# Kernel optimization log

Hardware: AMD Instinct MI355X
Metric: run time of the kernel (lower is better)

## Reference

```python
import jax, jax.numpy as jnp
import numpy as np

SIGMA = 1.0
NUM_CLASSES = 10


def setup_inputs() -> dict:
    key = jax.random.key(0)
    k1, k2, k3, k4 = jax.random.split(key, 4)
    ns, nt, d = 4096, 4096, 256
    return {
        "source_feature": jax.random.normal(k1, (ns, d), dtype=jnp.float32),
        "source_label": jax.random.randint(k2, (ns,), 0, NUM_CLASSES),
        "target_feature": jax.random.normal(k3, (nt, d), dtype=jnp.float32),
        "class_weight": jax.random.uniform(k4, (NUM_CLASSES,), dtype=jnp.float32),
    }


def _rbf_gram(x, y, sigma):
    # K[i, j] = exp(-||x_i - y_j||^2 / (2*sigma)); [n, m]
    x2 = jnp.sum(x * x, axis=-1)  # [n]
    y2 = jnp.sum(y * y, axis=-1)  # [m]
    sq = x2[:, None] + y2[None, :] - 2.0 * (x @ y.T)
    sq = jnp.maximum(sq, 0.0)
    return jnp.exp(-sq / (2.0 * sigma))


def reference(source_feature, source_label, target_feature, class_weight):
    ns = source_feature.shape[0]
    nt = target_feature.shape[0]
    w = class_weight[source_label]          # [ns] per-sample weight
    n = jnp.sum(w)                          # weighted source count

    Kss = _rbf_gram(source_feature, source_feature, SIGMA)  # [ns, ns]
    Ktt = _rbf_gram(target_feature, target_feature, SIGMA)  # [nt, nt]
    Kst = _rbf_gram(source_feature, target_feature, SIGMA)  # [ns, nt]

    first = jnp.einsum('i,ij,j->', w, Kss, w)
    sec = jnp.sum(Ktt)
    third = jnp.einsum('i,ij->', w, Kst)

    return first / (n * n) + sec / (nt * nt) - 2.0 * third / (n * nt)
```

## Files before the change

kernel.cpp:

```cpp
#include <hip/hip_runtime.h>
#include <hip/hip_bf16.h>


typedef float f32x4 __attribute__((ext_vector_type(4)));

#define D 256

static __device__ __forceinline__ unsigned char f32_to_e4m3(float f) {
    unsigned int u = __float_as_uint(f);
    unsigned int sg = (u >> 24) & 0x80;
    unsigned int um = u & 0x7FFFFFFF;
    unsigned int r = um + 0x0007FFFF + ((um >> 20) & 1);
    int e8 = (int)((r >> 23) & 0xFF) - 127 + 7;
    unsigned int m8 = (r >> 20) & 7;
    if (e8 <= 0) return (unsigned char)sg;
    if (e8 > 15 || (e8 == 15 && m8 == 7))
        return (unsigned char)(sg | 0x7E);
    return (unsigned char)(sg | ((unsigned)e8 << 3) | m8);
}


__global__ __launch_bounds__(256) void prep_kernel(
    const float* __restrict__ sf, const float* __restrict__ tf,
    const int* __restrict__ lbl, const float* __restrict__ cw,
    unsigned char* __restrict__ sfb, unsigned char* __restrict__ tfb,
    float* __restrict__ x2s, float* __restrict__ x2t,
    float* __restrict__ wv, int ns)
{
    int row = blockIdx.x * 4 + (threadIdx.x >> 6);
    int t = threadIdx.x & 63;
    bool is_src = row < ns;
    int r = is_src ? row : row - ns;
    const float* src = (is_src ? sf : tf) + (size_t)r * D;
    unsigned char* dstb = is_src ? sfb : tfb;

    float4 v = ((const float4*)src)[t];
    uchar4 q;
    q.x = f32_to_e4m3(v.x); q.y = f32_to_e4m3(v.y);
    q.z = f32_to_e4m3(v.z); q.w = f32_to_e4m3(v.w);

    int g = r >> 4, rr = r & 15;
    int s_ = t >> 3;
    int kg = (t >> 1) & 3;
    int j0 = (t & 1) * 4;
    size_t idx = ((size_t)(g * 8 + s_) * 512) + (size_t)(rr + 16 * kg) * 8 + j0;
    *(uchar4*)(dstb + idx) = q;

    float s = v.x * v.x + v.y * v.y + v.z * v.z + v.w * v.w;
    #pragma unroll
    for (int o = 32; o; o >>= 1) s += __shfl_xor(s, o);

    if (t == 0) {
        if (is_src) { wv[r] = cw[lbl[r]]; x2s[r] = s; }
        else        { x2t[r] = s; }
    }
}

__global__ __launch_bounds__(256, 3) void gram_kernel(
    const unsigned char* __restrict__ sfb, const unsigned char* __restrict__ tfb,
    const float* __restrict__ x2s, const float* __restrict__ x2t,
    const float* __restrict__ wv, float* __restrict__ bout,
    int ti_s, int ti_t)
{
    int tri_s = ti_s * (ti_s + 1) / 2;
    int tri_t = ti_t * (ti_t + 1) / 2;
    int blk = blockIdx.x;

    int mode, bi, bj;
    const unsigned char *X, *Y;
    const float *x2xp, *x2yp;
    if (blk < tri_s + tri_t) {
        int T, idx;
        if (blk < tri_s) { mode = 0; idx = blk; T = ti_s; X = sfb; Y = sfb; x2xp = x2s; x2yp = x2s; }
        else { mode = 1; idx = blk - tri_s; T = ti_t; X = tfb; Y = tfb; x2xp = x2t; x2yp = x2t; }
        bi = (int)((2.0f * T + 1.0f -
                    sqrtf((float)((2 * T + 1) * (2 * T + 1) - 8 * idx))) * 0.5f);
        if (bi < 0) bi = 0;
        if (bi > T - 1) bi = T - 1;
        int base = bi * (2 * T - bi + 1) / 2;
        while (base > idx) { --bi; base = bi * (2 * T - bi + 1) / 2; }
        while (idx >= base + (T - bi)) { base += (T - bi); ++bi; }
        bj = bi + (idx - base);
    } else {
        int idx = blk - tri_s - tri_t;
        mode = 2; bi = idx / ti_t; bj = idx % ti_t;
        X = sfb; Y = tfb; x2xp = x2s; x2yp = x2t;
    }
    float factor = (mode != 2 && bi != bj) ? 2.0f : 1.0f;

    int wid = threadIdx.x >> 6;
    int lane = threadIdx.x & 63;
    int wr = wid >> 1, wc = wid & 1;
    int R0 = bi * 128 + wr * 64;
    int C0 = bj * 128 + wc * 64;

    const unsigned char* XA = X + (size_t)(R0 >> 4) * 4096 + lane * 8;
    const unsigned char* YB = Y + (size_t)(C0 >> 4) * 4096 + lane * 8;

    f32x4 acc[4][4] = {};
    long af[4][4], bf_[4][4];
    #pragma unroll
    for (int sp = 0; sp < 3; ++sp) {
        #pragma unroll
        for (int m = 0; m < 4; ++m) {
            af[sp][m]  = *(const long*)(XA + (size_t)(m * 8 + sp) * 512);
            bf_[sp][m] = *(const long*)(YB + (size_t)(m * 8 + sp) * 512);
        }
    }
    #pragma unroll
    for (int s = 0; s < 8; ++s) {
        const int cur = s & 3;
        if (s < 5) {
            const int pf = (s + 3) & 3;
            #pragma unroll
            for (int m = 0; m < 4; ++m) {
                af[pf][m]  = *(const long*)(XA + (size_t)(m * 8 + s + 3) * 512);
                bf_[pf][m] = *(const long*)(YB + (size_t)(m * 8 + s + 3) * 512);
            }
        }
        #pragma unroll
        for (int m = 0; m < 4; ++m)
            #pragma unroll
            for (int n = 0; n < 4; ++n)
                acc[m][n] = __builtin_amdgcn_mfma_f32_16x16x32_fp8_fp8(
                    af[cur][m], bf_[cur][n], acc[m][n], 0, 0, 0);
    }

    int crow = (lane >> 4) * 4;
    int ccol = lane & 15;
    float x2yc[4];
    #pragma unroll
    for (int n = 0; n < 4; ++n) x2yc[n] = x2yp[C0 + 16 * n + ccol];

    float s = 0.0f;
    #pragma unroll
    for (int m = 0; m < 4; ++m) {
        #pragma unroll
        for (int r = 0; r < 4; ++r) {
            int gr = R0 + 16 * m + crow + r;
            float rx2 = x2xp[gr];
            float sq0 = fmaxf(rx2 + x2yc[0] - 2.0f * acc[m][0][r], 0.0f);
            float sq1 = fmaxf(rx2 + x2yc[1] - 2.0f * acc[m][1][r], 0.0f);
            float sq2 = fmaxf(rx2 + x2yc[2] - 2.0f * acc[m][2][r], 0.0f);
            float sq3 = fmaxf(rx2 + x2yc[3] - 2.0f * acc[m][3][r], 0.0f);
            float mn = fminf(fminf(sq0, sq1), fminf(sq2, sq3));
            if (__any(mn < 180.0f)) {
                float rw = (mode != 1) ? wv[gr] : 1.0f;
                float sqv[4] = {sq0, sq1, sq2, sq3};
                #pragma unroll
                for (int n = 0; n < 4; ++n) {
                    int gc = C0 + 16 * n + ccol;
                    float K = __expf(-0.5f * sqv[n]);
                    if (mode != 2 && gr == gc) K = 0.0f;
                    float wf = (mode == 0) ? rw * wv[gc] : rw;
                    s += wf * K;
                }
            }
        }
    }
    s *= factor;
    #pragma unroll
    for (int o = 32; o; o >>= 1) s += __shfl_xor(s, o);

    __shared__ float bsum[4];
    if (lane == 0) bsum[wid] = s;
    __syncthreads();
    if (threadIdx.x == 0)
        bout[blk] = (bsum[0] + bsum[1]) + (bsum[2] + bsum[3]);
}

__global__ __launch_bounds__(1024) void reduce_kernel(
    const float* __restrict__ wv, int ns,
    const float* __restrict__ bout, int tri_s, int tri_t, int nb,
    float* __restrict__ out, int nt)
{
    int tid = threadIdx.x;
    float n = 0.0f, dsq = 0.0f, a0 = 0.0f, a1 = 0.0f, a2 = 0.0f;
    for (int i = tid; i < ns; i += 1024) {
        float w = wv[i];
        n += w;
        dsq += w * w;
    }
    for (int i = tid; i < nb; i += 1024) {
        float v = bout[i];
        if (i < tri_s) a0 += v;
        else if (i < tri_s + tri_t) a1 += v;
        else a2 += v;
    }
    #pragma unroll
    for (int o = 32; o; o >>= 1) {
        n   += __shfl_xor(n, o);
        dsq += __shfl_xor(dsq, o);
        a0  += __shfl_xor(a0, o);
        a1  += __shfl_xor(a1, o);
        a2  += __shfl_xor(a2, o);
    }
    __shared__ float ln[16], ld[16], l0[16], l1[16], l2[16];
    int w = tid >> 6;
    if ((tid & 63) == 0) { ln[w] = n; ld[w] = dsq; l0[w] = a0; l1[w] = a1; l2[w] = a2; }
    __syncthreads();
    if (tid == 0) {
        float N = 0, DQ = 0, A0 = 0, A1 = 0, A2 = 0;
        #pragma unroll
        for (int i = 0; i < 16; ++i) {
            N += ln[i]; DQ += ld[i]; A0 += l0[i]; A1 += l1[i]; A2 += l2[i];
        }
        float fnt = (float)nt;
        out[0] = (A0 + DQ) / (N * N) + (A1 + fnt) / (fnt * fnt)
               - 2.0f * A2 / (N * fnt);
    }
}

extern "C" void kernel_launch(void* const* d_in, const int* in_sizes, int n_in,
                              void* d_out, int out_size, void* d_ws, size_t ws_size,
                              hipStream_t stream) {
    const float* sf = (const float*)d_in[0];
    const int* lbl = (const int*)d_in[1];
    const float* tf = (const float*)d_in[2];
    const float* cw = (const float*)d_in[3];
    float* out = (float*)d_out;

    int ns = in_sizes[1];
    int d = in_sizes[0] / ns;
    int nt = in_sizes[2] / d;

    char* p = (char*)d_ws;
    unsigned char* sfb = (unsigned char*)p;  p += (size_t)ns * d;
    unsigned char* tfb = (unsigned char*)p;  p += (size_t)nt * d;
    float* x2s = (float*)p;                  p += (size_t)ns * sizeof(float);
    float* x2t = (float*)p;                  p += (size_t)nt * sizeof(float);
    float* wv  = (float*)p;                  p += (size_t)ns * sizeof(float);
    float* bout = (float*)p;

    prep_kernel<<<(ns + nt) / 4, 256, 0, stream>>>(sf, tf, lbl, cw, sfb, tfb,
                                                   x2s, x2t, wv, ns);

    int ti_s = ns / 128, ti_t = nt / 128;
    int tri_s = ti_s * (ti_s + 1) / 2;
    int tri_t = ti_t * (ti_t + 1) / 2;
    int nblocks = tri_s + tri_t + ti_s * ti_t;
    gram_kernel<<<nblocks, 256, 0, stream>>>(sfb, tfb, x2s, x2t, wv, bout,
                                             ti_s, ti_t);

    reduce_kernel<<<1, 1024, 0, stream>>>(wv, ns, bout, tri_s, tri_t, nblocks,
                                          out, nt);
}
```

Measured before the change: 41.76 us.

## Batch gram tiles per block with XCD-aware mapping and wider fp8 loads

The gram kernel now processes four consecutive 128x128 tiles per block, assigned through an XCD-aware remap so neighbouring tiles share an XCD's L2. Per-mode partial sums go to a 3-wide output array. The fp8 packed layout is changed so each lane loads 16 bytes per step, halving the number of global load instructions. The prep kernel stages a 16-row group in LDS and writes it out with coalesced nontemporal 16-byte stores. The aims are to cut launch and tail overhead, raise cache reuse, and reduce load instruction count. The cost is fewer blocks (about 2080 → 520), which may lower occupancy and load balance.

```diff
diff --git a/kernel.cpp b/kernel.cpp
--- a/kernel.cpp
+++ b/kernel.cpp
@@ -3,20 +3,21 @@
 
 
 typedef float f32x4 __attribute__((ext_vector_type(4)));
+typedef long long2v __attribute__((ext_vector_type(2)));
+typedef unsigned int u32x4 __attribute__((ext_vector_type(4)));
 
 #define D 256
 
-static __device__ __forceinline__ unsigned char f32_to_e4m3(float f) {
+static __device__ __forceinline__ unsigned int f32_to_e4m3(float f) {
     unsigned int u = __float_as_uint(f);
     unsigned int sg = (u >> 24) & 0x80;
     unsigned int um = u & 0x7FFFFFFF;
     unsigned int r = um + 0x0007FFFF + ((um >> 20) & 1);
     int e8 = (int)((r >> 23) & 0xFF) - 127 + 7;
     unsigned int m8 = (r >> 20) & 7;
-    if (e8 <= 0) return (unsigned char)sg;
-    if (e8 > 15 || (e8 == 15 && m8 == 7))
-        return (unsigned char)(sg | 0x7E);
-    return (unsigned char)(sg | ((unsigned)e8 << 3) | m8);
+    if (e8 <= 0) return sg;
+    if (e8 > 15 || (e8 == 15 && m8 == 7)) return sg | 0x7E;
+    return sg | ((unsigned)e8 << 3) | m8;
 }
 
 
@@ -27,52 +28,65 @@
     float* __restrict__ x2s, float* __restrict__ x2t,
     float* __restrict__ wv, int ns)
 {
-    int row = blockIdx.x * 4 + (threadIdx.x >> 6);
-    int t = threadIdx.x & 63;
-    bool is_src = row < ns;
-    int r = is_src ? row : row - ns;
-    const float* src = (is_src ? sf : tf) + (size_t)r * D;
-    unsigned char* dstb = is_src ? sfb : tfb;
-
-    float4 v = ((const float4*)src)[t];
-    uchar4 q;
-    q.x = f32_to_e4m3(v.x); q.y = f32_to_e4m3(v.y);
-    q.z = f32_to_e4m3(v.z); q.w = f32_to_e4m3(v.w);
-
-    int g = r >> 4, rr = r & 15;
-    int s_ = t >> 3;
-    int kg = (t >> 1) & 3;
-    int j0 = (t & 1) * 4;
-    size_t idx = ((size_t)(g * 8 + s_) * 512) + (size_t)(rr + 16 * kg) * 8 + j0;
-    *(uchar4*)(dstb + idx) = q;
-
-    float s = v.x * v.x + v.y * v.y + v.z * v.z + v.w * v.w;
+    __shared__ unsigned int ldsb[1024];
+
+    int gb = blockIdx.x;
+    int nsg = ns >> 4;
+    bool is_src = gb < nsg;
+    int gloc = is_src ? gb : gb - nsg;
+    const float* src = (is_src ? sf : tf) + (size_t)gloc * 16 * D;
+    unsigned char* dstb = (is_src ? sfb : tfb) + (size_t)gloc * 4096;
+
+    int tid = threadIdx.x;
+    int l = tid & 63;
+    int w = tid >> 6;
+
+    if (is_src && tid < 16) {
+        int r = gloc * 16 + tid;
+        wv[r] = cw[lbl[r]];
+    }
+
     #pragma unroll
-    for (int o = 32; o; o >>= 1) s += __shfl_xor(s, o);
-
-    if (t == 0) {
-        if (is_src) { wv[r] = cw[lbl[r]]; x2s[r] = s; }
-        else        { x2t[r] = s; }
-    }
-}
-
-__global__ __launch_bounds__(256, 3) void gram_kernel(
-    const unsigned char* __restrict__ sfb, const unsigned char* __restrict__ tfb,
-    const float* __restrict__ x2s, const float* __restrict__ x2t,
-    const float* __restrict__ wv, float* __restrict__ bout,
-    int ti_s, int ti_t)
+    for (int p = 0; p < 4; ++p) {
+        int row = 4 * p + w;
+        int k0 = l * 4;
+        float4 v = *(const float4*)(src + row * D + k0);
+        unsigned int packed = f32_to_e4m3(v.x)
+                            | (f32_to_e4m3(v.y) << 8)
+                            | (f32_to_e4m3(v.z) << 16)
+                            | (f32_to_e4m3(v.w) << 24);
+        int s  = k0 >> 5;
+        int kg = (k0 >> 3) & 3;
+        int off = (s >> 1) * 1024 + (row + 16 * kg) * 16 + (s & 1) * 8 + (k0 & 7);
+        ldsb[off >> 2] = packed;
+
+        float ps = v.x * v.x + v.y * v.y + v.z * v.z + v.w * v.w;
+        #pragma unroll
+        for (int o = 32; o; o >>= 1) ps += __shfl_xor(ps, o);
+        if (l == 0) {
+            int gr = gloc * 16 + row;
+            if (is_src) x2s[gr] = ps; else x2t[gr] = ps;
+        }
+    }
+    __syncthreads();
+    u32x4 val = ((const u32x4*)ldsb)[tid];
+    __builtin_nontemporal_store(val, ((u32x4*)dstb) + tid);
+}
+
+static __device__ __forceinline__ void decode_tile(
+    int blk, int ti_s, int ti_t,
+    const unsigned char* sfb, const unsigned char* tfb,
+    const float* x2s, const float* x2t,
+    int& mode, int& bi, int& bj,
+    const unsigned char*& X, const unsigned char*& Y,
+    const float*& x2x, const float*& x2y, float& factor)
 {
     int tri_s = ti_s * (ti_s + 1) / 2;
     int tri_t = ti_t * (ti_t + 1) / 2;
-    int blk = blockIdx.x;
-
-    int mode, bi, bj;
-    const unsigned char *X, *Y;
-    const float *x2xp, *x2yp;
     if (blk < tri_s + tri_t) {
         int T, idx;
-        if (blk < tri_s) { mode = 0; idx = blk; T = ti_s; X = sfb; Y = sfb; x2xp = x2s; x2yp = x2s; }
-        else { mode = 1; idx = blk - tri_s; T = ti_t; X = tfb; Y = tfb; x2xp = x2t; x2yp = x2t; }
+        if (blk < tri_s) { mode = 0; idx = blk; T = ti_s; X = sfb; Y = sfb; x2x = x2s; x2y = x2s; }
+        else { mode = 1; idx = blk - tri_s; T = ti_t; X = tfb; Y = tfb; x2x = x2t; x2y = x2t; }
         bi = (int)((2.0f * T + 1.0f -
                     sqrtf((float)((2 * T + 1) * (2 * T + 1) - 8 * idx))) * 0.5f);
         if (bi < 0) bi = 0;
@@ -84,94 +98,126 @@
     } else {
         int idx = blk - tri_s - tri_t;
         mode = 2; bi = idx / ti_t; bj = idx % ti_t;
-        X = sfb; Y = tfb; x2xp = x2s; x2yp = x2t;
-    }
-    float factor = (mode != 2 && bi != bj) ? 2.0f : 1.0f;
+        X = sfb; Y = tfb; x2x = x2s; x2y = x2t;
+    }
+    factor = (mode != 2 && bi != bj) ? 2.0f : 1.0f;
+}
+
+__global__ __launch_bounds__(256, 3) void gram_kernel(
+    const unsigned char* __restrict__ sfb, const unsigned char* __restrict__ tfb,
+    const float* __restrict__ x2s, const float* __restrict__ x2t,
+    const float* __restrict__ wv, float* __restrict__ bout,
+    int ti_s, int ti_t, int NT, int NB, int TPB)
+{
+    int orig = blockIdx.x;
+    int q = NB >> 3, rm = NB & 7, xcd = orig & 7, of = orig >> 3;
+    int lb = (xcd < rm ? xcd * (q + 1) : rm * (q + 1) + (xcd - rm) * q) + of;
+    int tbeg = lb * TPB;
+    int tend = min(tbeg + TPB, NT);
 
     int wid = threadIdx.x >> 6;
     int lane = threadIdx.x & 63;
     int wr = wid >> 1, wc = wid & 1;
-    int R0 = bi * 128 + wr * 64;
-    int C0 = bj * 128 + wc * 64;
-
-    const unsigned char* XA = X + (size_t)(R0 >> 4) * 4096 + lane * 8;
-    const unsigned char* YB = Y + (size_t)(C0 >> 4) * 4096 + lane * 8;
-
-    f32x4 acc[4][4] = {};
-    long af[4][4], bf_[4][4];
-    #pragma unroll
-    for (int sp = 0; sp < 3; ++sp) {
-        #pragma unroll
-        for (int m = 0; m < 4; ++m) {
-            af[sp][m]  = *(const long*)(XA + (size_t)(m * 8 + sp) * 512);
-            bf_[sp][m] = *(const long*)(YB + (size_t)(m * 8 + sp) * 512);
-        }
-    }
-    #pragma unroll
-    for (int s = 0; s < 8; ++s) {
-        const int cur = s & 3;
-        if (s < 5) {
-            const int pf = (s + 3) & 3;
-            #pragma unroll
-            for (int m = 0; m < 4; ++m) {
-                af[pf][m]  = *(const long*)(XA + (size_t)(m * 8 + s + 3) * 512);
-                bf_[pf][m] = *(const long*)(YB + (size_t)(m * 8 + s + 3) * 512);
-            }
-        }
-        #pragma unroll
-        for (int m = 0; m < 4; ++m)
-            #pragma unroll
-            for (int n = 0; n < 4; ++n)
-                acc[m][n] = __builtin_amdgcn_mfma_f32_16x16x32_fp8_fp8(
-                    af[cur][m], bf_[cur][n], acc[m][n], 0, 0, 0);
-    }
-
     int crow = (lane >> 4) * 4;
     int ccol = lane & 15;
-    float x2yc[4];
-    #pragma unroll
-    for (int n = 0; n < 4; ++n) x2yc[n] = x2yp[C0 + 16 * n + ccol];
-
-    float s = 0.0f;
-    #pragma unroll
-    for (int m = 0; m < 4; ++m) {
-        #pragma unroll
-        for (int r = 0; r < 4; ++r) {
-            int gr = R0 + 16 * m + crow + r;
-            float rx2 = x2xp[gr];
-            float sq0 = fmaxf(rx2 + x2yc[0] - 2.0f * acc[m][0][r], 0.0f);
-            float sq1 = fmaxf(rx2 + x2yc[1] - 2.0f * acc[m][1][r], 0.0f);
-            float sq2 = fmaxf(rx2 + x2yc[2] - 2.0f * acc[m][2][r], 0.0f);
-            float sq3 = fmaxf(rx2 + x2yc[3] - 2.0f * acc[m][3][r], 0.0f);
-            float mn = fminf(fminf(sq0, sq1), fminf(sq2, sq3));
-            if (__any(mn < 180.0f)) {
-                float rw = (mode != 1) ? wv[gr] : 1.0f;
-                float sqv[4] = {sq0, sq1, sq2, sq3};
+
+    float s0 = 0.0f, s1 = 0.0f, s2 = 0.0f;
+
+    for (int t = tbeg; t < tend; ++t) {
+        int mode, bi, bj; float factor;
+        const unsigned char *X, *Y; const float *x2xp, *x2yp;
+        decode_tile(t, ti_s, ti_t, sfb, tfb, x2s, x2t,
+                    mode, bi, bj, X, Y, x2xp, x2yp, factor);
+
+        int R0 = bi * 128 + wr * 64;
+        int C0 = bj * 128 + wc * 64;
+        const unsigned char* XA = X + (size_t)(R0 >> 4) * 4096 + lane * 16;
+        const unsigned char* YB = Y + (size_t)(C0 >> 4) * 4096 + lane * 16;
+
+        f32x4 acc[4][4] = {};
+        long2v a2[2][4], b2[2][4];
+        #pragma unroll
+        for (int m = 0; m < 4; ++m) {
+            a2[0][m] = *(const long2v*)(XA + m * 4096);
+            b2[0][m] = *(const long2v*)(YB + m * 4096);
+        }
+        #pragma unroll
+        for (int ss = 0; ss < 4; ++ss) {
+            const int cur = ss & 1;
+            if (ss < 3) {
                 #pragma unroll
-                for (int n = 0; n < 4; ++n) {
-                    int gc = C0 + 16 * n + ccol;
-                    float K = __expf(-0.5f * sqv[n]);
-                    if (mode != 2 && gr == gc) K = 0.0f;
-                    float wf = (mode == 0) ? rw * wv[gc] : rw;
-                    s += wf * K;
+                for (int m = 0; m < 4; ++m) {
+                    a2[cur ^ 1][m] = *(const long2v*)(XA + m * 4096 + (ss + 1) * 1024);
+                    b2[cur ^ 1][m] = *(const long2v*)(YB + m * 4096 + (ss + 1) * 1024);
                 }
             }
-        }
-    }
-    s *= factor;
+            #pragma unroll
+            for (int m = 0; m < 4; ++m)
+                #pragma unroll
+                for (int n = 0; n < 4; ++n)
+                    acc[m][n] = __builtin_amdgcn_mfma_f32_16x16x32_fp8_fp8(
+                        a2[cur][m][0], b2[cur][n][0], acc[m][n], 0, 0, 0);
+            #pragma unroll
+            for (int m = 0; m < 4; ++m)
+                #pragma unroll
+                for (int n = 0; n < 4; ++n)
+                    acc[m][n] = __builtin_amdgcn_mfma_f32_16x16x32_fp8_fp8(
+                        a2[cur][m][1], b2[cur][n][1], acc[m][n], 0, 0, 0);
+        }
+
+        float x2yc[4];
+        #pragma unroll
+        for (int n = 0; n < 4; ++n) x2yc[n] = x2yp[C0 + 16 * n + ccol];
+
+        float s = 0.0f;
+        #pragma unroll
+        for (int m = 0; m < 4; ++m) {
+            #pragma unroll
+            for (int r = 0; r < 4; ++r) {
+                int gr = R0 + 16 * m + crow + r;
+                float rx2 = x2xp[gr];
+                float sq0 = fmaxf(rx2 + x2yc[0] - 2.0f * acc[m][0][r], 0.0f);
+                float sq1 = fmaxf(rx2 + x2yc[1] - 2.0f * acc[m][1][r], 0.0f);
+                float sq2 = fmaxf(rx2 + x2yc[2] - 2.0f * acc[m][2][r], 0.0f);
+                float sq3 = fmaxf(rx2 + x2yc[3] - 2.0f * acc[m][3][r], 0.0f);
+                float mn = fminf(fminf(sq0, sq1), fminf(sq2, sq3));
+                if (__any(mn < 180.0f)) {
+                    float rw = (mode != 1) ? wv[gr] : 1.0f;
+                    float sqv[4] = {sq0, sq1, sq2, sq3};
+                    #pragma unroll
+                    for (int n = 0; n < 4; ++n) {
+                        int gc = C0 + 16 * n + ccol;
+                        float K = __expf(-0.5f * sqv[n]);
+                        if (mode != 2 && gr == gc) K = 0.0f;
+                        float wf = (mode == 0) ? rw * wv[gc] : rw;
+                        s += wf * K;
+                    }
+                }
+            }
+        }
+        s *= factor;
+        if (mode == 0) s0 += s; else if (mode == 1) s1 += s; else s2 += s;
+    }
+
     #pragma unroll
-    for (int o = 32; o; o >>= 1) s += __shfl_xor(s, o);
-
-    __shared__ float bsum[4];
-    if (lane == 0) bsum[wid] = s;
+    for (int o = 32; o; o >>= 1) {
+        s0 += __shfl_xor(s0, o);
+        s1 += __shfl_xor(s1, o);
+        s2 += __shfl_xor(s2, o);
+    }
+    __shared__ float bsum[4][3];
+    if (lane == 0) { bsum[wid][0] = s0; bsum[wid][1] = s1; bsum[wid][2] = s2; }
     __syncthreads();
-    if (threadIdx.x == 0)
-        bout[blk] = (bsum[0] + bsum[1]) + (bsum[2] + bsum[3]);
+    if (threadIdx.x < 3) {
+        float v = bsum[0][threadIdx.x] + bsum[1][threadIdx.x]
+                + bsum[2][threadIdx.x] + bsum[3][threadIdx.x];
+        bout[orig * 3 + threadIdx.x] = v;
+    }
 }
 
 __global__ __launch_bounds__(1024) void reduce_kernel(
     const float* __restrict__ wv, int ns,
-    const float* __restrict__ bout, int tri_s, int tri_t, int nb,
+    const float* __restrict__ bout, int NB,
     float* __restrict__ out, int nt)
 {
     int tid = threadIdx.x;
@@ -181,11 +227,10 @@
         n += w;
         dsq += w * w;
     }
-    for (int i = tid; i < nb; i += 1024) {
-        float v = bout[i];
-        if (i < tri_s) a0 += v;
-        else if (i < tri_s + tri_t) a1 += v;
-        else a2 += v;
+    for (int i = tid; i < NB; i += 1024) {
+        a0 += bout[i * 3 + 0];
+        a1 += bout[i * 3 + 1];
+        a2 += bout[i * 3 + 2];
     }
     #pragma unroll
     for (int o = 32; o; o >>= 1) {
@@ -232,16 +277,17 @@
     float* wv  = (float*)p;                  p += (size_t)ns * sizeof(float);
     float* bout = (float*)p;
 
-    prep_kernel<<<(ns + nt) / 4, 256, 0, stream>>>(sf, tf, lbl, cw, sfb, tfb,
-                                                   x2s, x2t, wv, ns);
+    prep_kernel<<<(ns + nt) / 16, 256, 0, stream>>>(sf, tf, lbl, cw, sfb, tfb,
+                                                    x2s, x2t, wv, ns);
 
     int ti_s = ns / 128, ti_t = nt / 128;
     int tri_s = ti_s * (ti_s + 1) / 2;
     int tri_t = ti_t * (ti_t + 1) / 2;
-    int nblocks = tri_s + tri_t + ti_s * ti_t;
-    gram_kernel<<<nblocks, 256, 0, stream>>>(sfb, tfb, x2s, x2t, wv, bout,
-                                             ti_s, ti_t);
-
-    reduce_kernel<<<1, 1024, 0, stream>>>(wv, ns, bout, tri_s, tri_t, nblocks,
-                                          out, nt);
-}
+    int NT = tri_s + tri_t + ti_s * ti_t;
+    int TPB = 4;
+    int NB = (NT + TPB - 1) / TPB;
+    gram_kernel<<<NB, 256, 0, stream>>>(sfb, tfb, x2s, x2t, wv, bout,
+                                        ti_s, ti_t, NT, NB, TPB);
+
+    reduce_kernel<<<1, 1024, 0, stream>>>(wv, ns, bout, NB, out, nt);
+}
```

Measured after the change: 49.32 us. +18.1%, slower.

## Stage FP8 prep through LDS and split gram tiles across eight waves

Applied to the files above, without the earlier changes.

The prep kernel now handles a 16-row group per block. It packs FP8 values into LDS and writes them out with coalesced 16-byte nontemporal stores, replacing the scattered 4-byte writes. The gram kernel uses 512 threads (8 waves), with each wave computing a 64x32 subtile instead of 64x64. The prefetch ring shrinks from depth 3 to a double buffer. This raises wave-level parallelism and lowers register pressure per wave, at the cost of more redundant A-fragment loads and less prefetch depth.

```diff
diff --git a/kernel.cpp b/kernel.cpp
--- a/kernel.cpp
+++ b/kernel.cpp
@@ -3,20 +3,20 @@
 
 
 typedef float f32x4 __attribute__((ext_vector_type(4)));
+typedef unsigned int u32x4 __attribute__((ext_vector_type(4)));
 
 #define D 256
 
-static __device__ __forceinline__ unsigned char f32_to_e4m3(float f) {
+static __device__ __forceinline__ unsigned int f32_to_e4m3(float f) {
     unsigned int u = __float_as_uint(f);
     unsigned int sg = (u >> 24) & 0x80;
     unsigned int um = u & 0x7FFFFFFF;
     unsigned int r = um + 0x0007FFFF + ((um >> 20) & 1);
     int e8 = (int)((r >> 23) & 0xFF) - 127 + 7;
     unsigned int m8 = (r >> 20) & 7;
-    if (e8 <= 0) return (unsigned char)sg;
-    if (e8 > 15 || (e8 == 15 && m8 == 7))
-        return (unsigned char)(sg | 0x7E);
-    return (unsigned char)(sg | ((unsigned)e8 << 3) | m8);
+    if (e8 <= 0) return sg;
+    if (e8 > 15 || (e8 == 15 && m8 == 7)) return sg | 0x7E;
+    return sg | ((unsigned)e8 << 3) | m8;
 }
 
 
@@ -27,36 +27,52 @@
     float* __restrict__ x2s, float* __restrict__ x2t,
     float* __restrict__ wv, int ns)
 {
-    int row = blockIdx.x * 4 + (threadIdx.x >> 6);
-    int t = threadIdx.x & 63;
-    bool is_src = row < ns;
-    int r = is_src ? row : row - ns;
-    const float* src = (is_src ? sf : tf) + (size_t)r * D;
-    unsigned char* dstb = is_src ? sfb : tfb;
-
-    float4 v = ((const float4*)src)[t];
-    uchar4 q;
-    q.x = f32_to_e4m3(v.x); q.y = f32_to_e4m3(v.y);
-    q.z = f32_to_e4m3(v.z); q.w = f32_to_e4m3(v.w);
-
-    int g = r >> 4, rr = r & 15;
-    int s_ = t >> 3;
-    int kg = (t >> 1) & 3;
-    int j0 = (t & 1) * 4;
-    size_t idx = ((size_t)(g * 8 + s_) * 512) + (size_t)(rr + 16 * kg) * 8 + j0;
-    *(uchar4*)(dstb + idx) = q;
-
-    float s = v.x * v.x + v.y * v.y + v.z * v.z + v.w * v.w;
-    #pragma unroll
-    for (int o = 32; o; o >>= 1) s += __shfl_xor(s, o);
-
-    if (t == 0) {
-        if (is_src) { wv[r] = cw[lbl[r]]; x2s[r] = s; }
-        else        { x2t[r] = s; }
-    }
-}
-
-__global__ __launch_bounds__(256, 3) void gram_kernel(
+    __shared__ unsigned int ldsb[1024];
+
+    int gb = blockIdx.x;
+    int nsg = ns >> 4;
+    bool is_src = gb < nsg;
+    int gloc = is_src ? gb : gb - nsg;
+    const float* src = (is_src ? sf : tf) + (size_t)gloc * 16 * D;
+    unsigned char* dstb = (is_src ? sfb : tfb) + (size_t)gloc * 4096;
+
+    int tid = threadIdx.x;
+    int l = tid & 63;
+    int w = tid >> 6;
+
+    if (is_src && tid < 16) {
+        int r = gloc * 16 + tid;
+        wv[r] = cw[lbl[r]];
+    }
+
+    #pragma unroll
+    for (int p = 0; p < 4; ++p) {
+        int row = 4 * p + w;
+        int k0 = l * 4;
+        float4 v = *(const float4*)(src + row * D + k0);
+        unsigned int packed = f32_to_e4m3(v.x)
+                            | (f32_to_e4m3(v.y) << 8)
+                            | (f32_to_e4m3(v.z) << 16)
+                            | (f32_to_e4m3(v.w) << 24);
+        int s  = l >> 3;
+        int kg = (l >> 1) & 3;
+        int off = s * 512 + (row + 16 * kg) * 8 + (l & 1) * 4;
+        ldsb[off >> 2] = packed;
+
+        float ps = v.x * v.x + v.y * v.y + v.z * v.z + v.w * v.w;
+        #pragma unroll
+        for (int o = 32; o; o >>= 1) ps += __shfl_xor(ps, o);
+        if (l == 0) {
+            int gr = gloc * 16 + row;
+            if (is_src) x2s[gr] = ps; else x2t[gr] = ps;
+        }
+    }
+    __syncthreads();
+    u32x4 val = ((const u32x4*)ldsb)[tid];
+    __builtin_nontemporal_store(val, ((u32x4*)dstb) + tid);
+}
+
+__global__ __launch_bounds__(512, 4) void gram_kernel(
     const unsigned char* __restrict__ sfb, const unsigned char* __restrict__ tfb,
     const float* __restrict__ x2s, const float* __restrict__ x2t,
     const float* __restrict__ wv, float* __restrict__ bout,
@@ -90,47 +106,44 @@
 
     int wid = threadIdx.x >> 6;
     int lane = threadIdx.x & 63;
-    int wr = wid >> 1, wc = wid & 1;
+    int wr = wid >> 2, wc = wid & 3;
     int R0 = bi * 128 + wr * 64;
-    int C0 = bj * 128 + wc * 64;
-
-    const unsigned char* XA = X + (size_t)(R0 >> 4) * 4096 + lane * 8;
-    const unsigned char* YB = Y + (size_t)(C0 >> 4) * 4096 + lane * 8;
-
-    f32x4 acc[4][4] = {};
-    long af[4][4], bf_[4][4];
-    #pragma unroll
-    for (int sp = 0; sp < 3; ++sp) {
-        #pragma unroll
-        for (int m = 0; m < 4; ++m) {
-            af[sp][m]  = *(const long*)(XA + (size_t)(m * 8 + sp) * 512);
-            bf_[sp][m] = *(const long*)(YB + (size_t)(m * 8 + sp) * 512);
-        }
-    }
+    int C0 = bj * 128 + wc * 32;
+
+    const unsigned char* XA = X + (size_t)(bi * 8 + wr * 4) * 4096 + lane * 8;
+    const unsigned char* YB = Y + (size_t)(bj * 8 + wc * 2) * 4096 + lane * 8;
+
+    f32x4 acc[4][2] = {};
+    long af[2][4], bf_[2][2];
+    #pragma unroll
+    for (int m = 0; m < 4; ++m) af[0][m] = *(const long*)(XA + m * 4096);
+    #pragma unroll
+    for (int n = 0; n < 2; ++n) bf_[0][n] = *(const long*)(YB + n * 4096);
+
     #pragma unroll
     for (int s = 0; s < 8; ++s) {
-        const int cur = s & 3;
-        if (s < 5) {
-            const int pf = (s + 3) & 3;
+        const int cur = s & 1;
+        if (s < 7) {
             #pragma unroll
-            for (int m = 0; m < 4; ++m) {
-                af[pf][m]  = *(const long*)(XA + (size_t)(m * 8 + s + 3) * 512);
-                bf_[pf][m] = *(const long*)(YB + (size_t)(m * 8 + s + 3) * 512);
-            }
+            for (int m = 0; m < 4; ++m)
+                af[cur ^ 1][m] = *(const long*)(XA + m * 4096 + (s + 1) * 512);
+            #pragma unroll
+            for (int n = 0; n < 2; ++n)
+                bf_[cur ^ 1][n] = *(const long*)(YB + n * 4096 + (s + 1) * 512);
         }
         #pragma unroll
         for (int m = 0; m < 4; ++m)
             #pragma unroll
-            for (int n = 0; n < 4; ++n)
+            for (int n = 0; n < 2; ++n)
                 acc[m][n] = __builtin_amdgcn_mfma_f32_16x16x32_fp8_fp8(
                     af[cur][m], bf_[cur][n], acc[m][n], 0, 0, 0);
     }
 
     int crow = (lane >> 4) * 4;
     int ccol = lane & 15;
-    float x2yc[4];
-    #pragma unroll
-    for (int n = 0; n < 4; ++n) x2yc[n] = x2yp[C0 + 16 * n + ccol];
+    float x2yc[2];
+    #pragma unroll
+    for (int n = 0; n < 2; ++n) x2yc[n] = x2yp[C0 + 16 * n + ccol];
 
     float s = 0.0f;
     #pragma unroll
@@ -141,14 +154,12 @@
             float rx2 = x2xp[gr];
             float sq0 = fmaxf(rx2 + x2yc[0] - 2.0f * acc[m][0][r], 0.0f);
             float sq1 = fmaxf(rx2 + x2yc[1] - 2.0f * acc[m][1][r], 0.0f);
-            float sq2 = fmaxf(rx2 + x2yc[2] - 2.0f * acc[m][2][r], 0.0f);
-            float sq3 = fmaxf(rx2 + x2yc[3] - 2.0f * acc[m][3][r], 0.0f);
-            float mn = fminf(fminf(sq0, sq1), fminf(sq2, sq3));
+            float mn = fminf(sq0, sq1);
             if (__any(mn < 180.0f)) {
                 float rw = (mode != 1) ? wv[gr] : 1.0f;
-                float sqv[4] = {sq0, sq1, sq2, sq3};
+                float sqv[2] = {sq0, sq1};
                 #pragma unroll
-                for (int n = 0; n < 4; ++n) {
+                for (int n = 0; n < 2; ++n) {
                     int gc = C0 + 16 * n + ccol;
                     float K = __expf(-0.5f * sqv[n]);
                     if (mode != 2 && gr == gc) K = 0.0f;
@@ -162,11 +173,15 @@
     #pragma unroll
     for (int o = 32; o; o >>= 1) s += __shfl_xor(s, o);
 
-    __shared__ float bsum[4];
+    __shared__ float bsum[8];
     if (lane == 0) bsum[wid] = s;
     __syncthreads();
-    if (threadIdx.x == 0)
-        bout[blk] = (bsum[0] + bsum[1]) + (bsum[2] + bsum[3]);
+    if (threadIdx.x == 0) {
+        float t0 = 0.0f;
+        #pragma unroll
+        for (int i = 0; i < 8; ++i) t0 += bsum[i];
+        bout[blk] = t0;
+    }
 }
 
 __global__ __launch_bounds__(1024) void reduce_kernel(
@@ -232,14 +247,14 @@
     float* wv  = (float*)p;                  p += (size_t)ns * sizeof(float);
     float* bout = (float*)p;
 
-    prep_kernel<<<(ns + nt) / 4, 256, 0, stream>>>(sf, tf, lbl, cw, sfb, tfb,
-                                                   x2s, x2t, wv, ns);
+    prep_kernel<<<(ns + nt) / 16, 256, 0, stream>>>(sf, tf, lbl, cw, sfb, tfb,
+                                                    x2s, x2t, wv, ns);
 
     int ti_s = ns / 128, ti_t = nt / 128;
     int tri_s = ti_s * (ti_s + 1) / 2;
     int tri_t = ti_t * (ti_t + 1) / 2;
     int nblocks = tri_s + tri_t + ti_s * ti_t;
-    gram_kernel<<<nblocks, 256, 0, stream>>>(sfb, tfb, x2s, x2t, wv, bout,
+    gram_kernel<<<nblocks, 512, 0, stream>>>(sfb, tfb, x2s, x2t, wv, bout,
                                              ti_s, ti_t);
 
     reduce_kernel<<<1, 1024, 0, stream>>>(wv, ns, bout, tri_s, tri_t, nblocks,
```

New measurement: 51.54 us. +23.4%, slower.
